# Performance work log

Measured on AMD Instinct MI355X. Metric: run time of the kernel, lower is better.

The kernel has to match this reference:

```python
import jax, jax.numpy as jnp
import numpy as np

N = 100000   # nodes
E = 600000   # edges
D = 128      # d_model / hidden_dim
L = 4        # num_layers
V = 5000     # node vocab (in_size)
G = 128      # num graphs in batch
C = 10       # num_class
BN_EPS = 1e-5


def setup_inputs() -> dict:
    key = jax.random.key(0)
    ks = jax.random.split(key, 20)
    s = 0.05
    return {
        "x": jax.random.randint(ks[0], (N,), 0, V),
        "edge_index": jax.random.randint(ks[1], (2, E), 0, N),
        "edge_attr": jax.random.normal(ks[2], (E, 2), dtype=jnp.float32),
        "batch": jnp.sort(jax.random.randint(ks[3], (N,), 0, G)),
        # embedding table
        "emb": jax.random.normal(ks[4], (V, D), dtype=jnp.float32) * s,
        # per-layer GINEConv edge linear (edge_dim=2 -> D)
        "edge_w": jax.random.normal(ks[5], (L, 2, D), dtype=jnp.float32) * s,
        "edge_b": jnp.zeros((L, D), jnp.float32),
        # per-layer MLP: Linear -> BN -> ReLU -> Linear
        "w1": jax.random.normal(ks[6], (L, D, D), dtype=jnp.float32) * s,
        "b1": jnp.zeros((L, D), jnp.float32),
        "g1": jnp.ones((L, D), jnp.float32),
        "beta1": jnp.zeros((L, D), jnp.float32),
        "w2": jax.random.normal(ks[7], (L, D, D), dtype=jnp.float32) * s,
        "b2": jnp.zeros((L, D), jnp.float32),
        # per-layer outer BatchNorm (self.norms)
        "ng": jnp.ones((L, D), jnp.float32),
        "nb": jnp.zeros((L, D), jnp.float32),
        # classifier: Linear(D,D) -> ReLU -> Linear(D,C)
        "cw1": jax.random.normal(ks[8], (D, D), dtype=jnp.float32) * s,
        "cb1": jnp.zeros((D,), jnp.float32),
        "cw2": jax.random.normal(ks[9], (D, C), dtype=jnp.float32) * s,
        "cb2": jnp.zeros((C,), jnp.float32),
    }


def _bn(h, g, b):
    # training-mode BatchNorm1d over node axis, biased variance
    m = h.mean(0)
    v = h.var(0)
    return (h - m) * jax.lax.rsqrt(v + BN_EPS) * g + b


def reference(x, edge_index, edge_attr, batch, emb, edge_w, edge_b,
              w1, b1, g1, beta1, w2, b2, ng, nb, cw1, cb1, cw2, cb2):
    h = emb[x]                                    # [N, D]
    src, dst = edge_index[0], edge_index[1]
    for l in range(L):
        e = edge_attr @ edge_w[l] + edge_b[l]     # [E, D]
        msg = jax.nn.relu(h[src] + e)             # gather + add + relu
        agg = jax.ops.segment_sum(msg, dst, num_segments=N)  # scatter-sum
        z = h + agg                               # (1+eps)*x_i + aggr, eps=0
        z = jax.nn.relu(_bn(z @ w1[l] + b1[l], g1[l], beta1[l]))
        h = _bn(z @ w2[l] + b2[l], ng[l], nb[l])
        if l != L - 1:
            h = jax.nn.relu(h)
    sums = jax.ops.segment_sum(h, batch, num_segments=G)            # [G, D]
    counts = jax.ops.segment_sum(jnp.ones((N, 1), h.dtype), batch, num_segments=G)
    pooled = sums / jnp.maximum(counts, 1.0)      # global mean pool
    return jax.nn.relu(pooled @ cw1 + cb1) @ cw2 + cb2  # [G, C]
```

## Files before the change

### kernel.cpp

```cpp
#include <hip/hip_runtime.h>
#include <stdint.h>

#define N_NODES 100000
#define N_EDGES 600000
#define DMODEL  128
#define NLAYERS 4
#define NGRAPH  128
#define NCLASS  10
#define BN_EPS  1e-5f
#define NSLOT   32
#define STATSZ  (NSLOT * 2 * DMODEL)
#define ZSTR    136

typedef __bf16 bf16x8 __attribute__((ext_vector_type(8)));
typedef __bf16 bf16x4 __attribute__((ext_vector_type(4)));
typedef __bf16 bf16x2 __attribute__((ext_vector_type(2)));
typedef float  f32x4  __attribute__((ext_vector_type(4)));

__global__ void k_init(int* __restrict__ deg, float* __restrict__ statA,
                       float* __restrict__ statB, float* __restrict__ psum,
                       const float* __restrict__ w1, const float* __restrict__ w2,
                       __bf16* __restrict__ wt_hi, __bf16* __restrict__ wt_lo,
                       const int* __restrict__ batch, int* __restrict__ gstart) {
  int i = blockIdx.x * 256 + threadIdx.x;
  if (i < N_NODES) deg[i] = 0;
  if (i < NLAYERS * STATSZ) {
    statA[i] = 0.0f;
    statB[i] = 0.0f;
  }
  if (i < NGRAPH * DMODEL) psum[i] = 0.0f;
  {
    int mat = i >> 14;
    int rem = i & 16383;
    int n = rem >> 7;
    int k = rem & 127;
    int l = mat >> 1;
    int which = mat & 1;
    const float* w = which ? w2 : w1;
    float v = w[(size_t)l * DMODEL * DMODEL + (size_t)k * DMODEL + n];
    __bf16 hi = (__bf16)v;
    wt_hi[i] = hi;
    wt_lo[i] = (__bf16)(v - (float)hi);
  }
  if (i <= NGRAPH) {
    int lo = 0;
    int hi = N_NODES;
    while (lo < hi) {
      int mid = (lo + hi) >> 1;
      if (batch[mid] < i) lo = mid + 1; else hi = mid;
    }
    gstart[i] = lo;
  }
}

__global__ void k_embed(const int* __restrict__ x, const float* __restrict__ emb,
                        __bf16* __restrict__ h) {
  int idx = blockIdx.x * 256 + threadIdx.x;
  if (idx >= N_NODES * DMODEL / 8) return;
  int i = idx >> 4;
  int p = idx & 15;
  const float* src = emb + (size_t)x[i] * DMODEL + p * 8;
  float4 v0 = *(const float4*)(src);
  float4 v1 = *(const float4*)(src + 4);
  bf16x8 o;
  o[0] = (__bf16)v0.x; o[1] = (__bf16)v0.y; o[2] = (__bf16)v0.z; o[3] = (__bf16)v0.w;
  o[4] = (__bf16)v1.x; o[5] = (__bf16)v1.y; o[6] = (__bf16)v1.z; o[7] = (__bf16)v1.w;
  *(bf16x8*)(h + (size_t)i * DMODEL + p * 8) = o;
}

__global__ void k_hist(const int* __restrict__ dst, int* __restrict__ deg) {
  int e = blockIdx.x * 256 + threadIdx.x;
  if (e < N_EDGES) atomicAdd(&deg[dst[e]], 1);
}

__global__ void k_scan1(const int* __restrict__ deg, int* __restrict__ out,
                        int* __restrict__ bsum, int n) {
  __shared__ int lds[256];
  int t = threadIdx.x;
  int idx = blockIdx.x * 256 + t;
  int v = (idx < n) ? deg[idx] : 0;
  int val = v;
  lds[t] = val;
  for (int ofs = 1; ofs < 256; ofs <<= 1) {
    __syncthreads();
    int u = (t >= ofs) ? lds[t - ofs] : 0;
    __syncthreads();
    val += u;
    lds[t] = val;
  }
  if (idx < n) out[idx] = val - v;
  if (t == 255) bsum[blockIdx.x] = val;
}

__global__ void k_scan2(const int* __restrict__ bsum, int* __restrict__ bsumx, int nb) {
  __shared__ int lds[512];
  int t = threadIdx.x;
  int v = (t < nb) ? bsum[t] : 0;
  int val = v;
  lds[t] = val;
  for (int ofs = 1; ofs < 512; ofs <<= 1) {
    __syncthreads();
    int u = (t >= ofs) ? lds[t - ofs] : 0;
    __syncthreads();
    val += u;
    lds[t] = val;
  }
  if (t < nb) bsumx[t] = val - v;
}

__global__ void k_scan3(int* __restrict__ row_start, int* __restrict__ cursor,
                        const int* __restrict__ bsumx, int n, int total) {
  int idx = blockIdx.x * 256 + threadIdx.x;
  if (idx < n) {
    int v = row_start[idx] + bsumx[blockIdx.x];
    row_start[idx] = v;
    cursor[idx] = v;
  }
  if (idx == 0) row_start[n] = total;
}

__global__ void k_scatter(const int* __restrict__ ei, const float* __restrict__ ea,
                          int* __restrict__ cursor, int4* __restrict__ epack) {
  int e = blockIdx.x * 256 + threadIdx.x;
  if (e >= N_EDGES) return;
  int s = ei[e];
  int d = ei[N_EDGES + e];
  int pos = atomicAdd(&cursor[d], 1);
  int4 pk;
  pk.x = s;
  pk.y = __float_as_int(ea[2 * e]);
  pk.z = __float_as_int(ea[2 * e + 1]);
  pk.w = 0;
  epack[pos] = pk;
}

__global__ void __launch_bounds__(256) k_aggemm(
    const __bf16* __restrict__ h, const int* __restrict__ row_start,
    const int4* __restrict__ epack,
    const float* __restrict__ ew,
    const float* __restrict__ ebp,
    const float* __restrict__ statPrev,
    const float* __restrict__ gammaP, const float* __restrict__ betaP, int hasT,
    const __bf16* __restrict__ Whi, const __bf16* __restrict__ Wlo,
    const float* __restrict__ bias,
    __bf16* __restrict__ Y,
    float* __restrict__ statpart) {
  __shared__ __align__(16) __bf16 zt[32 * ZSTR];
  __shared__ float sld[DMODEL];
  __shared__ float tld[DMODEL];
  int tid = threadIdx.x;

  if (hasT) {
    if (tid < DMODEL) {
      float sum = 0.0f;
      float sq = 0.0f;
      for (int p = 0; p < NSLOT; ++p) {
        sum += statPrev[p * (2 * DMODEL) + tid];
        sq  += statPrev[p * (2 * DMODEL) + DMODEL + tid];
      }
      float mean = sum * (1.0f / N_NODES);
      float var = sq * (1.0f / N_NODES) - mean * mean;
      float inv = rsqrtf(var + BN_EPS);
      float s = gammaP[tid] * inv;
      sld[tid] = s;
      tld[tid] = betaP[tid] - mean * s;
    }
    __syncthreads();
  }

  int hw = tid >> 5;
  int ln = tid & 31;
  int d0 = ln * 4;

  float4 ew0 = *(const float4*)(ew + d0);
  float4 ew1 = *(const float4*)(ew + DMODEL + d0);
  float4 eb  = *(const float4*)(ebp + d0);
  float4 s4;
  float4 t4;
  if (hasT) {
    s4 = *(const float4*)(sld + d0);
    t4 = *(const float4*)(tld + d0);
  }

#define AGG_ONE(E, V)                                                          \
  {                                                                            \
    float a0 = __int_as_float((E).y);                                          \
    float a1 = __int_as_float((E).z);                                          \
    float f0 = (float)(V)[0];                                                  \
    float f1 = (float)(V)[1];                                                  \
    float f2 = (float)(V)[2];                                                  \
    float f3 = (float)(V)[3];                                                  \
    if (hasT) {                                                                \
      f0 = fmaxf(s4.x * f0 + t4.x, 0.0f);                                      \
      f1 = fmaxf(s4.y * f1 + t4.y, 0.0f);                                      \
      f2 = fmaxf(s4.z * f2 + t4.z, 0.0f);                                      \
      f3 = fmaxf(s4.w * f3 + t4.w, 0.0f);                                      \
    }                                                                          \
    acc0 += fmaxf(f0 + a0 * ew0.x + a1 * ew1.x + eb.x, 0.0f);                  \
    acc1 += fmaxf(f1 + a0 * ew0.y + a1 * ew1.y + eb.y, 0.0f);                  \
    acc2 += fmaxf(f2 + a0 * ew0.z + a1 * ew1.z + eb.z, 0.0f);                  \
    acc3 += fmaxf(f3 + a0 * ew0.w + a1 * ew1.w + eb.w, 0.0f);                  \
  }

  for (int i = 0; i < 4; ++i) {
    int nl = hw * 4 + i;
    int node = blockIdx.x * 32 + nl;
    bf16x4 hv = *(const bf16x4*)(h + (size_t)node * DMODEL + d0);
    float acc0, acc1, acc2, acc3;
    {
      float r0 = (float)hv[0];
      float r1 = (float)hv[1];
      float r2 = (float)hv[2];
      float r3 = (float)hv[3];
      if (hasT) {
        acc0 = fmaxf(s4.x * r0 + t4.x, 0.0f);
        acc1 = fmaxf(s4.y * r1 + t4.y, 0.0f);
        acc2 = fmaxf(s4.z * r2 + t4.z, 0.0f);
        acc3 = fmaxf(s4.w * r3 + t4.w, 0.0f);
      } else {
        acc0 = r0; acc1 = r1; acc2 = r2; acc3 = r3;
      }
    }
    int j0 = row_start[node];
    int j1 = row_start[node + 1];
    int j = j0;
    for (; j + 4 <= j1; j += 4) {
      int4 e0 = epack[j];
      int4 e1 = epack[j + 1];
      int4 e2 = epack[j + 2];
      int4 e3 = epack[j + 3];
      bf16x4 v0 = *(const bf16x4*)(h + (size_t)e0.x * DMODEL + d0);
      bf16x4 v1 = *(const bf16x4*)(h + (size_t)e1.x * DMODEL + d0);
      bf16x4 v2 = *(const bf16x4*)(h + (size_t)e2.x * DMODEL + d0);
      bf16x4 v3 = *(const bf16x4*)(h + (size_t)e3.x * DMODEL + d0);
      AGG_ONE(e0, v0)
      AGG_ONE(e1, v1)
      AGG_ONE(e2, v2)
      AGG_ONE(e3, v3)
    }
    for (; j < j1; ++j) {
      int4 e0 = epack[j];
      bf16x4 v0 = *(const bf16x4*)(h + (size_t)e0.x * DMODEL + d0);
      AGG_ONE(e0, v0)
    }
    bf16x4 o;
    o[0] = (__bf16)acc0;
    o[1] = (__bf16)acc1;
    o[2] = (__bf16)acc2;
    o[3] = (__bf16)acc3;
    *(bf16x4*)(zt + nl * ZSTR + d0) = o;
  }
#undef AGG_ONE

  __syncthreads();

  int wave = tid >> 6;
  int lane = tid & 63;
  int n16 = lane & 15;
  int quad = lane >> 4;

  bf16x8 bhi[2][4];
  bf16x8 blo[2][4];
#pragma unroll
  for (int ct = 0; ct < 2; ++ct) {
    int n = (wave * 2 + ct) * 16 + n16;
#pragma unroll
    for (int kk = 0; kk < 4; ++kk) {
      int k0 = kk * 32 + quad * 8;
      bhi[ct][kk] = *(const bf16x8*)(Whi + (size_t)n * DMODEL + k0);
      blo[ct][kk] = *(const bf16x8*)(Wlo + (size_t)n * DMODEL + k0);
    }
  }
  float bc[2];
  bc[0] = bias[(wave * 2 + 0) * 16 + n16];
  bc[1] = bias[(wave * 2 + 1) * 16 + n16];

  bf16x8 a[2][4];
#pragma unroll
  for (int t = 0; t < 2; ++t) {
    const __bf16* zr = zt + (t * 16 + n16) * ZSTR;
#pragma unroll
    for (int kk = 0; kk < 4; ++kk) {
      a[t][kk] = *(const bf16x8*)(zr + kk * 32 + quad * 8);
    }
  }

  f32x4 acc[2][2];
#pragma unroll
  for (int t = 0; t < 2; ++t)
#pragma unroll
    for (int ct = 0; ct < 2; ++ct)
#pragma unroll
      for (int r = 0; r < 4; ++r) acc[t][ct][r] = 0.0f;

#pragma unroll
  for (int kk = 0; kk < 4; ++kk) {
#pragma unroll
    for (int ct = 0; ct < 2; ++ct) {
#pragma unroll
      for (int t = 0; t < 2; ++t) {
        acc[t][ct] = __builtin_amdgcn_mfma_f32_16x16x32_bf16(a[t][kk], bhi[ct][kk], acc[t][ct], 0, 0, 0);
        acc[t][ct] = __builtin_amdgcn_mfma_f32_16x16x32_bf16(a[t][kk], blo[ct][kk], acc[t][ct], 0, 0, 0);
      }
    }
  }

  int row0 = blockIdx.x * 32;
  float ssum[2] = {0.0f, 0.0f};
  float ssq[2] = {0.0f, 0.0f};
#pragma unroll
  for (int t = 0; t < 2; ++t) {
#pragma unroll
    for (int ct = 0; ct < 2; ++ct) {
      int col = (wave * 2 + ct) * 16 + n16;
#pragma unroll
      for (int r = 0; r < 4; ++r) {
        int row = row0 + t * 16 + quad * 4 + r;
        float v = acc[t][ct][r] + bc[ct];
        Y[(size_t)row * DMODEL + col] = (__bf16)v;
        ssum[ct] += v;
        ssq[ct] += v * v;
      }
    }
  }

  int slot = blockIdx.x & (NSLOT - 1);
#pragma unroll
  for (int ct = 0; ct < 2; ++ct) {
    int col = (wave * 2 + ct) * 16 + n16;
    float s = ssum[ct];
    float q = ssq[ct];
    s += __shfl_xor(s, 16);
    q += __shfl_xor(q, 16);
    s += __shfl_xor(s, 32);
    q += __shfl_xor(q, 32);
    if (quad == 0) {
      atomicAdd(&statpart[slot * (2 * DMODEL) + col], s);
      atomicAdd(&statpart[slot * (2 * DMODEL) + DMODEL + col], q);
    }
  }
}

__global__ void __launch_bounds__(256) k_gemm2(
    const __bf16* __restrict__ X,
    const __bf16* __restrict__ Whi, const __bf16* __restrict__ Wlo,
    const float* __restrict__ bias,
    const float* __restrict__ statA,
    const float* __restrict__ gamma, const float* __restrict__ beta,
    __bf16* __restrict__ Y,
    float* __restrict__ statpart) {
  __shared__ float sld[DMODEL];
  __shared__ float tld[DMODEL];
  int tid = threadIdx.x;

  if (tid < DMODEL) {
    float sum = 0.0f;
    float sq = 0.0f;
    for (int p = 0; p < NSLOT; ++p) {
      sum += statA[p * (2 * DMODEL) + tid];
      sq  += statA[p * (2 * DMODEL) + DMODEL + tid];
    }
    float mean = sum * (1.0f / N_NODES);
    float var = sq * (1.0f / N_NODES) - mean * mean;
    float inv = rsqrtf(var + BN_EPS);
    float s = gamma[tid] * inv;
    sld[tid] = s;
    tld[tid] = beta[tid] - mean * s;
  }
  __syncthreads();

  int wave = tid >> 6;
  int lane = tid & 63;
  int n16 = lane & 15;
  int quad = lane >> 4;

  bf16x8 bhi[2][4];
  bf16x8 blo[2][4];
#pragma unroll
  for (int ct = 0; ct < 2; ++ct) {
    int n = (wave * 2 + ct) * 16 + n16;
#pragma unroll
    for (int kk = 0; kk < 4; ++kk) {
      int k0 = kk * 32 + quad * 8;
      bhi[ct][kk] = *(const bf16x8*)(Whi + (size_t)n * DMODEL + k0);
      blo[ct][kk] = *(const bf16x8*)(Wlo + (size_t)n * DMODEL + k0);
    }
  }
  float bc[2];
  bc[0] = bias[(wave * 2 + 0) * 16 + n16];
  bc[1] = bias[(wave * 2 + 1) * 16 + n16];

  float ssum[2] = {0.0f, 0.0f};
  float ssq[2] = {0.0f, 0.0f};

  const int NCHUNK = N_NODES / 32;
  for (int c = blockIdx.x; c < NCHUNK; c += gridDim.x) {
    int row0 = c * 32;
    bf16x8 a[2][4];
#pragma unroll
    for (int t = 0; t < 2; ++t) {
      const __bf16* xr = X + (size_t)(row0 + t * 16 + n16) * DMODEL;
#pragma unroll
      for (int kk = 0; kk < 4; ++kk) {
        a[t][kk] = *(const bf16x8*)(xr + kk * 32 + quad * 8);
      }
    }
#pragma unroll
    for (int kk = 0; kk < 4; ++kk) {
      int k0 = kk * 32 + quad * 8;
      float4 s0 = *(const float4*)(sld + k0);
      float4 s1 = *(const float4*)(sld + k0 + 4);
      float4 t0 = *(const float4*)(tld + k0);
      float4 t1 = *(const float4*)(tld + k0 + 4);
      float sv[8];
      float tv[8];
      sv[0] = s0.x; sv[1] = s0.y; sv[2] = s0.z; sv[3] = s0.w;
      sv[4] = s1.x; sv[5] = s1.y; sv[6] = s1.z; sv[7] = s1.w;
      tv[0] = t0.x; tv[1] = t0.y; tv[2] = t0.z; tv[3] = t0.w;
      tv[4] = t1.x; tv[5] = t1.y; tv[6] = t1.z; tv[7] = t1.w;
#pragma unroll
      for (int t = 0; t < 2; ++t) {
#pragma unroll
        for (int jj = 0; jj < 8; ++jj) {
          float f = (float)a[t][kk][jj];
          a[t][kk][jj] = (__bf16)fmaxf(sv[jj] * f + tv[jj], 0.0f);
        }
      }
    }

    f32x4 acc[2][2];
#pragma unroll
    for (int t = 0; t < 2; ++t)
#pragma unroll
      for (int ct = 0; ct < 2; ++ct)
#pragma unroll
        for (int r = 0; r < 4; ++r) acc[t][ct][r] = 0.0f;

#pragma unroll
    for (int kk = 0; kk < 4; ++kk) {
#pragma unroll
      for (int ct = 0; ct < 2; ++ct) {
#pragma unroll
        for (int t = 0; t < 2; ++t) {
          acc[t][ct] = __builtin_amdgcn_mfma_f32_16x16x32_bf16(a[t][kk], bhi[ct][kk], acc[t][ct], 0, 0, 0);
          acc[t][ct] = __builtin_amdgcn_mfma_f32_16x16x32_bf16(a[t][kk], blo[ct][kk], acc[t][ct], 0, 0, 0);
        }
      }
    }

#pragma unroll
    for (int t = 0; t < 2; ++t) {
#pragma unroll
      for (int ct = 0; ct < 2; ++ct) {
        int col = (wave * 2 + ct) * 16 + n16;
#pragma unroll
        for (int r = 0; r < 4; ++r) {
          int row = row0 + t * 16 + quad * 4 + r;
          float v = acc[t][ct][r] + bc[ct];
          Y[(size_t)row * DMODEL + col] = (__bf16)v;
          ssum[ct] += v;
          ssq[ct] += v * v;
        }
      }
    }
  }

  int slot = blockIdx.x & (NSLOT - 1);
#pragma unroll
  for (int ct = 0; ct < 2; ++ct) {
    int col = (wave * 2 + ct) * 16 + n16;
    float s = ssum[ct];
    float q = ssq[ct];
    s += __shfl_xor(s, 16);
    q += __shfl_xor(q, 16);
    s += __shfl_xor(s, 32);
    q += __shfl_xor(q, 32);
    if (quad == 0) {
      atomicAdd(&statpart[slot * (2 * DMODEL) + col], s);
      atomicAdd(&statpart[slot * (2 * DMODEL) + DMODEL + col], q);
    }
  }
}

__global__ void k_pool(const __bf16* __restrict__ h, const int* __restrict__ gstart,
                       float* __restrict__ psum) {
  int g = blockIdx.x;
  int slice = blockIdx.y;
  int lane = threadIdx.x;
  int d0 = lane * 2;
  int i0 = gstart[g];
  int i1 = gstart[g + 1];
  float a0 = 0.0f;
  float a1 = 0.0f;
  for (int i = i0 + slice; i < i1; i += 8) {
    bf16x2 v = *(const bf16x2*)(h + (size_t)i * DMODEL + d0);
    a0 += (float)v[0];
    a1 += (float)v[1];
  }
  atomicAdd(&psum[g * DMODEL + d0], a0);
  atomicAdd(&psum[g * DMODEL + d0 + 1], a1);
}

__global__ void k_classifier(const float* __restrict__ psum, const int* __restrict__ gstart,
                             const float* __restrict__ statB,
                             const float* __restrict__ gamma, const float* __restrict__ beta,
                             const float* __restrict__ cw1, const float* __restrict__ cb1,
                             const float* __restrict__ cw2, const float* __restrict__ cb2,
                             float* __restrict__ out) {
  __shared__ float pl[DMODEL];
  __shared__ float hid[DMODEL];
  int g = blockIdx.x;
  int d = threadIdx.x;
  float sum = 0.0f;
  float sq = 0.0f;
  for (int p = 0; p < NSLOT; ++p) {
    sum += statB[p * (2 * DMODEL) + d];
    sq  += statB[p * (2 * DMODEL) + DMODEL + d];
  }
  float mean = sum * (1.0f / N_NODES);
  float var = sq * (1.0f / N_NODES) - mean * mean;
  float inv = rsqrtf(var + BN_EPS);
  float s2 = gamma[d] * inv;
  float t2 = beta[d] - mean * s2;

  int cnt = gstart[g + 1] - gstart[g];
  pl[d] = (cnt > 0) ? (s2 * (psum[g * DMODEL + d] / (float)cnt) + t2) : 0.0f;
  __syncthreads();
  float acc = cb1[d];
  for (int k = 0; k < DMODEL; ++k) acc += pl[k] * cw1[k * DMODEL + d];
  hid[d] = fmaxf(acc, 0.0f);
  __syncthreads();
  if (d < NCLASS) {
    float acc2 = cb2[d];
    for (int k = 0; k < DMODEL; ++k) acc2 += hid[k] * cw2[k * NCLASS + d];
    out[g * NCLASS + d] = acc2;
  }
}

extern "C" void kernel_launch(void* const* d_in, const int* in_sizes, int n_in,
                              void* d_out, int out_size, void* d_ws, size_t ws_size,
                              hipStream_t stream) {
  const int*   x      = (const int*)d_in[0];
  const int*   ei     = (const int*)d_in[1];
  const float* ea     = (const float*)d_in[2];
  const int*   batch  = (const int*)d_in[3];
  const float* emb    = (const float*)d_in[4];
  const float* edge_w = (const float*)d_in[5];
  const float* edge_b = (const float*)d_in[6];
  const float* w1     = (const float*)d_in[7];
  const float* b1     = (const float*)d_in[8];
  const float* g1     = (const float*)d_in[9];
  const float* beta1  = (const float*)d_in[10];
  const float* w2     = (const float*)d_in[11];
  const float* b2     = (const float*)d_in[12];
  const float* ng     = (const float*)d_in[13];
  const float* nb     = (const float*)d_in[14];
  const float* cw1    = (const float*)d_in[15];
  const float* cb1    = (const float*)d_in[16];
  const float* cw2    = (const float*)d_in[17];
  const float* cb2    = (const float*)d_in[18];

  char* ws = (char*)d_ws;
  size_t off = 0;
  auto alloc = [&](size_t bytes) -> void* {
    void* p = ws + off;
    off += (bytes + 255) & ~(size_t)255;
    return p;
  };

  __bf16* h_bf      = (__bf16*)alloc((size_t)N_NODES * DMODEL * sizeof(__bf16));
  __bf16* y1_bf     = (__bf16*)alloc((size_t)N_NODES * DMODEL * sizeof(__bf16));
  int*    row_start = (int*)alloc((N_NODES + 1) * sizeof(int));
  int*    cursor    = (int*)alloc(N_NODES * sizeof(int));
  int*    deg       = (int*)alloc(N_NODES * sizeof(int));
  int4*   epack     = (int4*)alloc((size_t)N_EDGES * sizeof(int4));
  __bf16* wt_hi     = (__bf16*)alloc((size_t)NLAYERS * 2 * DMODEL * DMODEL * sizeof(__bf16));
  __bf16* wt_lo     = (__bf16*)alloc((size_t)NLAYERS * 2 * DMODEL * DMODEL * sizeof(__bf16));
  float*  statA     = (float*)alloc((size_t)NLAYERS * STATSZ * sizeof(float));
  float*  statB     = (float*)alloc((size_t)NLAYERS * STATSZ * sizeof(float));
  int*    gstart    = (int*)alloc((NGRAPH + 1) * sizeof(int));
  float*  psum      = (float*)alloc((size_t)NGRAPH * DMODEL * sizeof(float));
  int*    bsum      = (int*)alloc(512 * sizeof(int));
  int*    bsumx     = (int*)alloc(512 * sizeof(int));

  auto statAL = [&](int l) { return statA + (size_t)l * STATSZ; };
  auto statBL = [&](int l) { return statB + (size_t)l * STATSZ; };

  const int nbScan = (N_NODES + 255) / 256;
  const int nbEdge = (N_EDGES + 255) / 256;
  const int nbEmb  = (N_NODES * DMODEL / 8 + 255) / 256;
  const int nbGemm = 782;
  const int nbFuse = N_NODES / 32;

  k_init<<<512, 256, 0, stream>>>(deg, statA, statB, psum,
                                  w1, w2, wt_hi, wt_lo, batch, gstart);
  k_embed<<<nbEmb, 256, 0, stream>>>(x, emb, h_bf);
  k_hist<<<nbEdge, 256, 0, stream>>>(ei + N_EDGES, deg);
  k_scan1<<<nbScan, 256, 0, stream>>>(deg, row_start, bsum, N_NODES);
  k_scan2<<<1, 512, 0, stream>>>(bsum, bsumx, nbScan);
  k_scan3<<<nbScan, 256, 0, stream>>>(row_start, cursor, bsumx, N_NODES, N_EDGES);
  k_scatter<<<nbEdge, 256, 0, stream>>>(ei, ea, cursor, epack);

  for (int l = 0; l < NLAYERS; ++l) {
    const float* sPrev = (l > 0) ? statBL(l - 1) : (const float*)nullptr;
    const float* gPrev = (l > 0) ? (ng + (size_t)(l - 1) * DMODEL) : (const float*)nullptr;
    const float* bPrev = (l > 0) ? (nb + (size_t)(l - 1) * DMODEL) : (const float*)nullptr;
    k_aggemm<<<nbFuse, 256, 0, stream>>>(
        h_bf, row_start, epack,
        edge_w + (size_t)l * 2 * DMODEL,
        edge_b + (size_t)l * DMODEL,
        sPrev, gPrev, bPrev, (l > 0) ? 1 : 0,
        wt_hi + (size_t)(l * 2 + 0) * DMODEL * DMODEL,
        wt_lo + (size_t)(l * 2 + 0) * DMODEL * DMODEL,
        b1 + (size_t)l * DMODEL,
        y1_bf, statAL(l));
    k_gemm2<<<nbGemm, 256, 0, stream>>>(
        y1_bf,
        wt_hi + (size_t)(l * 2 + 1) * DMODEL * DMODEL,
        wt_lo + (size_t)(l * 2 + 1) * DMODEL * DMODEL,
        b2 + (size_t)l * DMODEL,
        statAL(l), g1 + (size_t)l * DMODEL, beta1 + (size_t)l * DMODEL,
        h_bf, statBL(l));
  }

  dim3 poolGrid(NGRAPH, 8);
  k_pool<<<poolGrid, 64, 0, stream>>>(h_bf, gstart, psum);
  k_classifier<<<NGRAPH, DMODEL, 0, stream>>>(psum, gstart, statBL(NLAYERS - 1),
                                              ng + (size_t)(NLAYERS - 1) * DMODEL,
                                              nb + (size_t)(NLAYERS - 1) * DMODEL,
                                              cw1, cb1, cw2, cb2, (float*)d_out);
}
```

Before: 664.0 us.

## Sort nodes by in-degree to balance work in fused aggregate-GEMM blocks

Adds a counting sort of nodes by in-degree (histogram, scan, scatter into a schedule array). The fused aggregation+GEMM kernel then processes nodes in that order and writes output rows back to their original indices. The aim is to cut load imbalance and divergence within blocks, where nodes with very different edge counts currently share a wave. In exchange it adds three small preprocessing kernels, indirect node indexing, and scattered row writes and h reads that lose locality.

```diff
diff --git a/kernel.cpp b/kernel.cpp
--- a/kernel.cpp
+++ b/kernel.cpp
@@ -11,6 +11,7 @@
 #define NSLOT   32
 #define STATSZ  (NSLOT * 2 * DMODEL)
 #define ZSTR    136
+#define NBIN    64
 
 typedef __bf16 bf16x8 __attribute__((ext_vector_type(8)));
 typedef __bf16 bf16x4 __attribute__((ext_vector_type(4)));
@@ -19,6 +20,7 @@
 
 __global__ void k_init(int* __restrict__ deg, float* __restrict__ statA,
                        float* __restrict__ statB, float* __restrict__ psum,
+                       int* __restrict__ dbin,
                        const float* __restrict__ w1, const float* __restrict__ w2,
                        __bf16* __restrict__ wt_hi, __bf16* __restrict__ wt_lo,
                        const int* __restrict__ batch, int* __restrict__ gstart) {
@@ -29,6 +31,7 @@
     statB[i] = 0.0f;
   }
   if (i < NGRAPH * DMODEL) psum[i] = 0.0f;
+  if (i < NBIN) dbin[i] = 0;
   {
     int mat = i >> 14;
     int rem = i & 16383;
@@ -134,9 +137,59 @@
   epack[pos] = pk;
 }
 
+__global__ void k_dhist(const int* __restrict__ deg, int* __restrict__ dbin) {
+  __shared__ int lbin[NBIN];
+  int t = threadIdx.x;
+  if (t < NBIN) lbin[t] = 0;
+  __syncthreads();
+  int i = blockIdx.x * 256 + t;
+  if (i < N_NODES) {
+    int b = min(deg[i], NBIN - 1);
+    atomicAdd(&lbin[b], 1);
+  }
+  __syncthreads();
+  if (t < NBIN && lbin[t] > 0) atomicAdd(&dbin[t], lbin[t]);
+}
+
+__global__ void k_dscan(const int* __restrict__ dbin, int* __restrict__ dcursor) {
+  __shared__ int lds[NBIN];
+  int t = threadIdx.x;
+  int v = dbin[t];
+  int val = v;
+  lds[t] = val;
+  for (int ofs = 1; ofs < NBIN; ofs <<= 1) {
+    __syncthreads();
+    int u = (t >= ofs) ? lds[t - ofs] : 0;
+    __syncthreads();
+    val += u;
+    lds[t] = val;
+  }
+  dcursor[t] = val - v;
+}
+
+__global__ void k_dscatter(const int* __restrict__ deg, int* __restrict__ dcursor,
+                           int* __restrict__ sched) {
+  __shared__ int lcnt[NBIN];
+  __shared__ int lbase[NBIN];
+  int t = threadIdx.x;
+  if (t < NBIN) lcnt[t] = 0;
+  __syncthreads();
+  int i = blockIdx.x * 256 + t;
+  int b = 0;
+  int lrank = 0;
+  if (i < N_NODES) {
+    b = min(deg[i], NBIN - 1);
+    lrank = atomicAdd(&lcnt[b], 1);
+  }
+  __syncthreads();
+  if (t < NBIN) lbase[t] = (lcnt[t] > 0) ? atomicAdd(&dcursor[t], lcnt[t]) : 0;
+  __syncthreads();
+  if (i < N_NODES) sched[lbase[b] + lrank] = i;
+}
+
 __global__ void __launch_bounds__(256) k_aggemm(
     const __bf16* __restrict__ h, const int* __restrict__ row_start,
-    const int4* __restrict__ epack,
+    const int4* __restrict__ epack, const int* __restrict__ sched,
     const float* __restrict__ ew,
     const float* __restrict__ ebp,
     const float* __restrict__ statPrev,
@@ -148,6 +201,7 @@
   __shared__ __align__(16) __bf16 zt[32 * ZSTR];
   __shared__ float sld[DMODEL];
   __shared__ float tld[DMODEL];
+  __shared__ int snode[32];
   int tid = threadIdx.x;
 
   if (hasT) {
@@ -204,7 +258,8 @@
 
   for (int i = 0; i < 4; ++i) {
     int nl = hw * 4 + i;
-    int node = blockIdx.x * 32 + nl;
+    int node = sched[blockIdx.x * 32 + nl];
+    if (ln == 0) snode[nl] = node;
     bf16x4 hv = *(const bf16x4*)(h + (size_t)node * DMODEL + d0);
     float acc0, acc1, acc2, acc3;
     {
@@ -305,7 +360,6 @@
     }
   }
 
-  int row0 = blockIdx.x * 32;
   float ssum[2] = {0.0f, 0.0f};
   float ssq[2] = {0.0f, 0.0f};
 #pragma unroll
@@ -315,7 +369,7 @@
       int col = (wave * 2 + ct) * 16 + n16;
 #pragma unroll
       for (int r = 0; r < 4; ++r) {
-        int row = row0 + t * 16 + quad * 4 + r;
+        int row = snode[t * 16 + quad * 4 + r];
         float v = acc[t][ct][r] + bc[ct];
         Y[(size_t)row * DMODEL + col] = (__bf16)v;
         ssum[ct] += v;
@@ -573,6 +627,7 @@
   int*    row_start = (int*)alloc((N_NODES + 1) * sizeof(int));
   int*    cursor    = (int*)alloc(N_NODES * sizeof(int));
   int*    deg       = (int*)alloc(N_NODES * sizeof(int));
+  int*    sched     = (int*)alloc(N_NODES * sizeof(int));
   int4*   epack     = (int4*)alloc((size_t)N_EDGES * sizeof(int4));
   __bf16* wt_hi     = (__bf16*)alloc((size_t)NLAYERS * 2 * DMODEL * DMODEL * sizeof(__bf16));
   __bf16* wt_lo     = (__bf16*)alloc((size_t)NLAYERS * 2 * DMODEL * DMODEL * sizeof(__bf16));
@@ -580,6 +635,8 @@
   float*  statB     = (float*)alloc((size_t)NLAYERS * STATSZ * sizeof(float));
   int*    gstart    = (int*)alloc((NGRAPH + 1) * sizeof(int));
   float*  psum      = (float*)alloc((size_t)NGRAPH * DMODEL * sizeof(float));
+  int*    dbin      = (int*)alloc(NBIN * sizeof(int));
+  int*    dcursor   = (int*)alloc(NBIN * sizeof(int));
   int*    bsum      = (int*)alloc(512 * sizeof(int));
   int*    bsumx     = (int*)alloc(512 * sizeof(int));
 
@@ -592,7 +649,7 @@
   const int nbGemm = 782;
   const int nbFuse = N_NODES / 32;
 
-  k_init<<<512, 256, 0, stream>>>(deg, statA, statB, psum,
+  k_init<<<512, 256, 0, stream>>>(deg, statA, statB, psum, dbin,
                                   w1, w2, wt_hi, wt_lo, batch, gstart);
   k_embed<<<nbEmb, 256, 0, stream>>>(x, emb, h_bf);
   k_hist<<<nbEdge, 256, 0, stream>>>(ei + N_EDGES, deg);
@@ -600,13 +657,16 @@
   k_scan2<<<1, 512, 0, stream>>>(bsum, bsumx, nbScan);
   k_scan3<<<nbScan, 256, 0, stream>>>(row_start, cursor, bsumx, N_NODES, N_EDGES);
   k_scatter<<<nbEdge, 256, 0, stream>>>(ei, ea, cursor, epack);
+  k_dhist<<<nbScan, 256, 0, stream>>>(deg, dbin);
+  k_dscan<<<1, NBIN, 0, stream>>>(dbin, dcursor);
+  k_dscatter<<<nbScan, 256, 0, stream>>>(deg, dcursor, sched);
 
   for (int l = 0; l < NLAYERS; ++l) {
     const float* sPrev = (l > 0) ? statBL(l - 1) : (const float*)nullptr;
     const float* gPrev = (l > 0) ? (ng + (size_t)(l - 1) * DMODEL) : (const float*)nullptr;
     const float* bPrev = (l > 0) ? (nb + (size_t)(l - 1) * DMODEL) : (const float*)nullptr;
     k_aggemm<<<nbFuse, 256, 0, stream>>>(
-        h_bf, row_start, epack,
+        h_bf, row_start, epack, sched,
         edge_w + (size_t)l * 2 * DMODEL,
         edge_b + (size_t)l * DMODEL,
         sPrev, gPrev, bPrev, (l > 0) ? 1 : 0,
```

New measurement: 660.8 us. No clear change (-0.5%).
